# Performance work log

Hardware: AMD Instinct MI355X
Metric: run time of the kernel (lower is better)

## Reference

```python
import jax, jax.numpy as jnp
import numpy as np

N = 50000          # nodes
E = 800000         # edges (before self loops)
IN_C = 128
HEADS = 4
D = 64             # out_per_head
HID = HEADS * D    # 256
OUT_C = 128
NEG_SLOPE = 0.2


def setup_inputs() -> dict:
    key = jax.random.key(0)
    ks = jax.random.split(key, 20)
    x = jax.random.normal(ks[0], (N, IN_C), dtype=jnp.float32)
    edge_index = jax.random.randint(ks[1], (2, E), 0, N, dtype=jnp.int32)
    s = 0.05
    params = {}
    dims = [IN_C, HID, HID]
    for i in range(3):
        params[f"W{i+1}"] = jax.random.normal(ks[2 + 4 * i], (dims[i], HID), dtype=jnp.float32) * s
        params[f"a_src{i+1}"] = jax.random.normal(ks[3 + 4 * i], (HEADS, D), dtype=jnp.float32) * s
        params[f"a_dst{i+1}"] = jax.random.normal(ks[4 + 4 * i], (HEADS, D), dtype=jnp.float32) * s
        params[f"b{i+1}"] = jnp.zeros((HID,), dtype=jnp.float32)
    params["head_W"] = jax.random.normal(ks[14], (HID, OUT_C), dtype=jnp.float32) * s
    params["head_b"] = jnp.zeros((OUT_C,), dtype=jnp.float32)
    return {"x": x, "edge_index": edge_index, **params}


def _gat_layer(x, src, dst, W, a_src, a_dst, b):
    # project: [N, heads, D]
    h = (x @ W).reshape(-1, HEADS, D)
    # per-node attention halves: [N, heads]
    alpha_s = jnp.einsum("nhd,hd->nh", h, a_src)
    alpha_d = jnp.einsum("nhd,hd->nh", h, a_dst)
    # per-edge logits: [E, heads]
    logits = jax.nn.leaky_relu(alpha_s[src] + alpha_d[dst], negative_slope=NEG_SLOPE)
    # segment softmax over incoming edges of each dst node
    seg_max = jax.ops.segment_max(logits, dst, num_segments=N)
    e = jnp.exp(logits - seg_max[dst])
    seg_sum = jax.ops.segment_sum(e, dst, num_segments=N)
    alpha = e / (seg_sum[dst] + 1e-16)
    # weighted messages, scatter-aggregate: [N, heads, D]
    msg = h[src] * alpha[:, :, None]
    out = jax.ops.segment_sum(msg, dst, num_segments=N)
    return out.reshape(-1, HID) + b


def reference(x, edge_index, W1, a_src1, a_dst1, b1, W2, a_src2, a_dst2, b2,
              W3, a_src3, a_dst3, b3, head_W, head_b):
    # add self loops once (add_self_loops=True in every GATConv)
    loop = jnp.arange(N, dtype=edge_index.dtype)
    src = jnp.concatenate([edge_index[0], loop])
    dst = jnp.concatenate([edge_index[1], loop])
    h = x
    layers = [(W1, a_src1, a_dst1, b1), (W2, a_src2, a_dst2, b2), (W3, a_src3, a_dst3, b3)]
    for (W, a_s, a_d, b) in layers:
        h = jax.nn.elu(_gat_layer(h, src, dst, W, a_s, a_d, b))
        # dropout inactive in eval mode
    graph_emb = jnp.mean(h, axis=0)          # global_mean_pool over single graph
    logits = graph_emb @ head_W + head_b     # [OUT_C]
    return logits
```

## Files before the change

kernel.cpp:

```cpp
#include <hip/hip_runtime.h>
#include <stdint.h>

#define NN 50000
#define EE 800000
#define ET 850000
#define INC 128
#define HID 256
#define OUTC 128
#define NB ((NN + 255) / 256)
#define GDEG ((ET + 255) / 256)
#define GTRP 640

typedef __attribute__((ext_vector_type(4))) float f32x4;
typedef __attribute__((ext_vector_type(8))) short s16x8;
typedef __attribute__((ext_vector_type(4))) short s16x4;

static __device__ __forceinline__ float b2f(unsigned short u){
  union { float f; unsigned int i; } v; v.i = ((unsigned int)u) << 16; return v.f;
}
static __device__ __forceinline__ unsigned short f2b(float f){
  union { float f; unsigned int i; } v; v.f = f;
  unsigned int r = v.i + 0x7FFFu + ((v.i >> 16) & 1u);
  return (unsigned short)(r >> 16);
}

__global__ void k_init(const int* __restrict__ ei, int* __restrict__ cnt,
                       const float* __restrict__ W1, const float* __restrict__ W2,
                       const float* __restrict__ W3, unsigned short* __restrict__ T1,
                       unsigned short* __restrict__ T2, unsigned short* __restrict__ T3,
                       float* __restrict__ pool){
  int b = blockIdx.x, tid = threadIdx.x;
  if (b < GDEG){
    int e = b * 256 + tid;
    if (e < ET){
      int d = (e < EE) ? ei[EE + e] : (e - EE);
      atomicAdd(&cnt[d], 1);
    }
  } else if (b < GDEG + GTRP){
    int bb = b - GDEG;
    const float* W; unsigned short* WT; int K, base;
    if (bb < 128)      { W = W1; WT = T1; K = 128; base = 0; }
    else if (bb < 384) { W = W2; WT = T2; K = 256; base = 128; }
    else               { W = W3; WT = T3; K = 256; base = 384; }
    int idx = (bb - base) * 256 + tid;
    int k = idx >> 8, c = idx & 255;
    WT[c * K + k] = f2b(W[idx]);
  } else {
    pool[tid] = 0.f;
  }
}

__global__ void k_blockscan(int* __restrict__ cnt, int* __restrict__ off,
                            int* __restrict__ bsum){
  __shared__ int s[256];
  int b = blockIdx.x, tid = threadIdx.x;
  int i = b * 256 + tid;
  int v = (i < NN) ? cnt[i] : 0;
  if (i < NN) cnt[i] = 0;
  s[tid] = v; __syncthreads();
  #pragma unroll
  for (int o = 1; o < 256; o <<= 1){
    int t = (tid >= o) ? s[tid - o] : 0; __syncthreads();
    s[tid] += t; __syncthreads();
  }
  if (i < NN) off[i] = s[tid] - v;
  if (tid == 255) bsum[b] = s[255];
}

__global__ void k_scanb(const int* __restrict__ bsum, int* __restrict__ bbase){
  __shared__ int s[256];
  int tid = threadIdx.x;
  int v = (tid < NB) ? bsum[tid] : 0;
  s[tid] = v; __syncthreads();
  #pragma unroll
  for (int o = 1; o < 256; o <<= 1){
    int t = (tid >= o) ? s[tid - o] : 0; __syncthreads();
    s[tid] += t; __syncthreads();
  }
  if (tid < NB) bbase[tid] = s[tid] - v;
}

__global__ void k_scatter(const int* __restrict__ ei, const int* __restrict__ off,
                          const int* __restrict__ bbase, int* __restrict__ cnt,
                          int* __restrict__ ssrc){
  int e = blockIdx.x * 256 + threadIdx.x;
  if (e >= ET) return;
  int s, d;
  if (e < EE){ s = ei[e]; d = ei[EE + e]; } else { s = e - EE; d = s; }
  int p = off[d] + bbase[d >> 8] + atomicAdd(&cnt[d], 1);
  ssrc[p] = s;
}

template<bool AF32>
__global__ __launch_bounds__(256) void k_gemm_fused(const void* __restrict__ Av,
    const unsigned short* __restrict__ WT,
    const float* __restrict__ a_src, const float* __restrict__ a_dst,
    unsigned short* __restrict__ C, float* __restrict__ as_, float* __restrict__ ad_,
    int M, int K){
  __shared__ unsigned short sA[2][32][72];
  int tid = threadIdx.x;
  int wave = tid >> 6, lane = tid & 63;
  int bm0 = blockIdx.x * 32;
  int wc0 = wave * 64;
  f32x4 acc[2][4];
  #pragma unroll
  for (int i = 0; i < 2; i++)
    #pragma unroll
    for (int j = 0; j < 4; j++) acc[i][j] = (f32x4){0.f, 0.f, 0.f, 0.f};

  s16x8 rg;
  int r0 = tid >> 3, kb0 = (tid & 7) * 8;

  auto ldA = [&](int k0){
    int gr = bm0 + r0;
    if constexpr (AF32){
      const float* A = (const float*)Av;
      unsigned short t[8] = {0,0,0,0,0,0,0,0};
      if (gr < M){
        const float4* p = (const float4*)(A + (size_t)gr * K + k0 + kb0);
        float4 v0 = p[0], v1 = p[1];
        t[0]=f2b(v0.x); t[1]=f2b(v0.y); t[2]=f2b(v0.z); t[3]=f2b(v0.w);
        t[4]=f2b(v1.x); t[5]=f2b(v1.y); t[6]=f2b(v1.z); t[7]=f2b(v1.w);
      }
      rg = *(s16x8*)t;
    } else {
      const unsigned short* A = (const unsigned short*)Av;
      s16x8 v = (s16x8){0,0,0,0,0,0,0,0};
      if (gr < M) v = *(const s16x8*)(A + (size_t)gr * K + k0 + kb0);
      rg = v;
    }
  };

  int T = K >> 6;
  ldA(0); *(s16x8*)&sA[0][r0][kb0] = rg;
  __syncthreads();
  for (int t = 0; t < T; t++){
    int k0 = t << 6;
    if (t + 1 < T) ldA(k0 + 64);
    int cur = t & 1;
    s16x8 af[2][2], bf[2][4];
    #pragma unroll
    for (int half = 0; half < 2; half++){
      int kl = half * 32 + (lane >> 4) * 8;
      af[half][0] = *(const s16x8*)&sA[cur][lane & 15][kl];
      af[half][1] = *(const s16x8*)&sA[cur][16 + (lane & 15)][kl];
      #pragma unroll
      for (int ni = 0; ni < 4; ni++)
        bf[half][ni] = *(const s16x8*)(WT + (size_t)(wc0 + ni * 16 + (lane & 15)) * K + k0 + kl);
    }
    #pragma unroll
    for (int half = 0; half < 2; half++)
      #pragma unroll
      for (int mi = 0; mi < 2; mi++)
        #pragma unroll
        for (int ni = 0; ni < 4; ni++)
          acc[mi][ni] = __builtin_amdgcn_mfma_f32_16x16x32_bf16(af[half][mi], bf[half][ni], acc[mi][ni], 0, 0, 0);
    if (t + 1 < T) *(s16x8*)&sA[cur ^ 1][r0][kb0] = rg;
    __syncthreads();
  }

  #pragma unroll
  for (int mi = 0; mi < 2; mi++){
    #pragma unroll
    for (int ni = 0; ni < 4; ni++){
      int col = wc0 + ni * 16 + (lane & 15);
      int rb = mi * 16 + (lane >> 4) * 4;
      #pragma unroll
      for (int r = 0; r < 4; r++){
        int row = rb + r;
        if (bm0 + row < M) C[(size_t)(bm0 + row) * HID + col] = f2b(acc[mi][ni][r]);
      }
    }
  }
  float asv[4], adv[4];
  #pragma unroll
  for (int ni = 0; ni < 4; ni++){
    int d = wc0 + ni * 16 + (lane & 15);
    asv[ni] = a_src[d];
    adv[ni] = a_dst[d];
  }
  #pragma unroll
  for (int mi = 0; mi < 2; mi++){
    #pragma unroll
    for (int r = 0; r < 4; r++){
      float ps = 0.f, pd = 0.f;
      #pragma unroll
      for (int ni = 0; ni < 4; ni++){
        float cv = acc[mi][ni][r];
        ps += cv * asv[ni];
        pd += cv * adv[ni];
      }
      #pragma unroll
      for (int m = 1; m < 16; m <<= 1){
        ps += __shfl_xor(ps, m, 64);
        pd += __shfl_xor(pd, m, 64);
      }
      int row = bm0 + mi * 16 + (lane >> 4) * 4 + r;
      if ((lane & 15) == 0 && row < M){
        as_[(size_t)row * 4 + wave] = ps;
        ad_[(size_t)row * 4 + wave] = pd;
      }
    }
  }
}

__global__ __launch_bounds__(256) void k_aggregate(const int* __restrict__ off,
    const int* __restrict__ bbase, const int* __restrict__ ssrc,
    const float* __restrict__ as_, const float* __restrict__ ad_,
    const unsigned short* __restrict__ h, const float* __restrict__ bias,
    unsigned short* __restrict__ out){
  int gid = blockIdx.x * 256 + threadIdx.x;
  int wid = gid >> 6, lane = gid & 63;
  if (wid >= NN) return;
  int start = off[wid] + bbase[wid >> 8];
  int end = (wid + 1 < NN) ? (off[wid + 1] + bbase[(wid + 1) >> 8]) : ET;
  int e1 = end - 1;
  int hq = lane >> 4;
  int hh = lane & 3;
  int el = lane >> 2;
  float ad_hh = ad_[(size_t)wid * 4 + hh];
  float ssum = 0.f;
  f32x4 acc = {0.f, 0.f, 0.f, 0.f};

  for (int base = start; base < end; base += 16){
    int nv = end - base; if (nv > 16) nv = 16;
    int sidx = ssrc[min(base + el, e1)];
    float lg = as_[(size_t)sidx * 4 + hh] + ad_hh;
    lg = fmaxf(lg, 0.2f * lg);
    float w = (el < nv) ? __expf(lg) : 0.f;
    int idxs[16];
    #pragma unroll
    for (int j = 0; j < 16; j++) idxs[j] = __shfl(sidx, j * 4, 64);
    s16x4 rows[16];
    #pragma unroll
    for (int j = 0; j < 16; j++){
      if (j < nv) rows[j] = *(const s16x4*)(h + (size_t)idxs[j] * HID + lane * 4);
    }
    #pragma unroll
    for (int j = 0; j < 16; j++){
      if (j < nv){
        float wj = __shfl(w, j * 4 + hq, 64);
        ssum += wj;
        #pragma unroll
        for (int c = 0; c < 4; c++) acc[c] += wj * b2f((unsigned short)rows[j][c]);
      }
    }
  }

  float inv = 1.f / (ssum + 1e-16f);
  float4 bv = *(const float4*)(bias + lane * 4);
  float o0 = acc[0] * inv + bv.x;
  float o1 = acc[1] * inv + bv.y;
  float o2 = acc[2] * inv + bv.z;
  float o3 = acc[3] * inv + bv.w;
  o0 = o0 > 0.f ? o0 : (__expf(o0) - 1.f);
  o1 = o1 > 0.f ? o1 : (__expf(o1) - 1.f);
  o2 = o2 > 0.f ? o2 : (__expf(o2) - 1.f);
  o3 = o3 > 0.f ? o3 : (__expf(o3) - 1.f);
  s16x4 ov;
  ov[0] = (short)f2b(o0); ov[1] = (short)f2b(o1);
  ov[2] = (short)f2b(o2); ov[3] = (short)f2b(o3);
  *(s16x4*)(out + (size_t)wid * HID + lane * 4) = ov;
}

__global__ __launch_bounds__(256) void k_pool(const unsigned short* __restrict__ X,
                                              float* __restrict__ pool){
  int b = blockIdx.x, c = threadIdx.x;
  int n0 = b * 64, n1 = min(n0 + 64, NN);
  float acc = 0.f;
  for (int n = n0; n < n1; n++) acc += b2f(X[(size_t)n * HID + c]);
  atomicAdd(&pool[c], acc);
}

__global__ void k_head(const float* __restrict__ pool, const float* __restrict__ hW,
                       const float* __restrict__ hb, float* __restrict__ outp){
  int o = threadIdx.x;
  float acc = hb[o];
  const float invN = 1.f / (float)NN;
  for (int c = 0; c < HID; c++) acc += pool[c] * invN * hW[c * OUTC + o];
  outp[o] = acc;
}

extern "C" void kernel_launch(void* const* d_in, const int* in_sizes, int n_in,
                              void* d_out, int out_size, void* d_ws, size_t ws_size,
                              hipStream_t stream){
  const float* x  = (const float*)d_in[0];
  const int* ei   = (const int*)d_in[1];
  const float* W[3]   = {(const float*)d_in[2],  (const float*)d_in[6],  (const float*)d_in[10]};
  const float* Asr[3] = {(const float*)d_in[3],  (const float*)d_in[7],  (const float*)d_in[11]};
  const float* Adt[3] = {(const float*)d_in[4],  (const float*)d_in[8],  (const float*)d_in[12]};
  const float* B[3]   = {(const float*)d_in[5],  (const float*)d_in[9],  (const float*)d_in[13]};
  const float* hW = (const float*)d_in[14];
  const float* hb = (const float*)d_in[15];

  char* w = (char*)d_ws; size_t o = 0;
  auto alloc = [&](size_t b) -> void* { void* p = w + o; o = (o + b + 255) & ~(size_t)255; return p; };
  int* cnt  = (int*)alloc((size_t)NN * 4);
  int* off  = (int*)alloc((size_t)NN * 4);
  int* ssrc = (int*)alloc((size_t)ET * 4);
  int* bsum = (int*)alloc((size_t)NB * 4);
  int* bbase= (int*)alloc((size_t)NB * 4);
  unsigned short* hbuf = (unsigned short*)alloc((size_t)NN * HID * 2);
  float* as_ = (float*)alloc((size_t)NN * 4 * 4);
  float* ad_ = (float*)alloc((size_t)NN * 4 * 4);
  unsigned short* X0 = (unsigned short*)alloc((size_t)NN * HID * 2);
  unsigned short* X1 = (unsigned short*)alloc((size_t)NN * HID * 2);
  unsigned short* WT1 = (unsigned short*)alloc((size_t)INC * HID * 2);
  unsigned short* WT2 = (unsigned short*)alloc((size_t)HID * HID * 2);
  unsigned short* WT3 = (unsigned short*)alloc((size_t)HID * HID * 2);
  float* pool = (float*)alloc(256 * 4);

  hipMemsetAsync(cnt, 0, (size_t)NN * 4, stream);
  k_init<<<GDEG + GTRP + 1, 256, 0, stream>>>(ei, cnt, W[0], W[1], W[2], WT1, WT2, WT3, pool);
  k_blockscan<<<NB, 256, 0, stream>>>(cnt, off, bsum);
  k_scanb<<<1, 256, 0, stream>>>(bsum, bbase);
  k_scatter<<<GDEG, 256, 0, stream>>>(ei, off, bbase, cnt, ssrc);

  const unsigned short* WTs[3] = {WT1, WT2, WT3};
  unsigned short* outbuf[3] = {X0, X1, X0};
  int Ks[3] = {INC, HID, HID};
  const void* Ain = (const void*)x;
  int gB = (NN + 63) / 64;
  int gG = (NN + 31) / 32;
  int gW = (NN * 64 + 255) / 256;
  for (int l = 0; l < 3; l++){
    if (l == 0) k_gemm_fused<true ><<<gG, 256, 0, stream>>>(Ain, WTs[l], Asr[l], Adt[l], hbuf, as_, ad_, NN, Ks[l]);
    else        k_gemm_fused<false><<<gG, 256, 0, stream>>>(Ain, WTs[l], Asr[l], Adt[l], hbuf, as_, ad_, NN, Ks[l]);
    k_aggregate<<<gW, 256, 0, stream>>>(off, bbase, ssrc, as_, ad_, hbuf, B[l], outbuf[l]);
    Ain = (const void*)outbuf[l];
  }
  k_pool<<<gB, 256, 0, stream>>>(X0, pool);
  k_head<<<1, 128, 0, stream>>>(pool, hW, hb, (float*)d_out);
}
```

Measured before the change: 441.1 us.

## Software-pipeline aggregation over two nodes per wave and record CSR slot in init

```diff
diff --git a/kernel.cpp b/kernel.cpp
--- a/kernel.cpp
+++ b/kernel.cpp
@@ -25,6 +25,7 @@
 }
 
 __global__ void k_init(const int* __restrict__ ei, int* __restrict__ cnt,
+                       int* __restrict__ pos,
                        const float* __restrict__ W1, const float* __restrict__ W2,
                        const float* __restrict__ W3, unsigned short* __restrict__ T1,
                        unsigned short* __restrict__ T2, unsigned short* __restrict__ T3,
@@ -34,7 +35,7 @@
     int e = b * 256 + tid;
     if (e < ET){
       int d = (e < EE) ? ei[EE + e] : (e - EE);
-      atomicAdd(&cnt[d], 1);
+      pos[e] = atomicAdd(&cnt[d], 1);
     }
   } else if (b < GDEG + GTRP){
     int bb = b - GDEG;
@@ -50,13 +51,12 @@
   }
 }
 
-__global__ void k_blockscan(int* __restrict__ cnt, int* __restrict__ off,
+__global__ void k_blockscan(const int* __restrict__ cnt, int* __restrict__ off,
                             int* __restrict__ bsum){
   __shared__ int s[256];
   int b = blockIdx.x, tid = threadIdx.x;
   int i = b * 256 + tid;
   int v = (i < NN) ? cnt[i] : 0;
-  if (i < NN) cnt[i] = 0;
   s[tid] = v; __syncthreads();
   #pragma unroll
   for (int o = 1; o < 256; o <<= 1){
@@ -81,14 +81,13 @@
 }
 
 __global__ void k_scatter(const int* __restrict__ ei, const int* __restrict__ off,
-                          const int* __restrict__ bbase, int* __restrict__ cnt,
+                          const int* __restrict__ bbase, const int* __restrict__ pos,
                           int* __restrict__ ssrc){
   int e = blockIdx.x * 256 + threadIdx.x;
   if (e >= ET) return;
   int s, d;
   if (e < EE){ s = ei[e]; d = ei[EE + e]; } else { s = e - EE; d = s; }
-  int p = off[d] + bbase[d >> 8] + atomicAdd(&cnt[d], 1);
-  ssrc[p] = s;
+  ssrc[off[d] + bbase[d >> 8] + pos[e]] = s;
 }
 
 template<bool AF32>
@@ -204,63 +203,134 @@
   }
 }
 
-__global__ __launch_bounds__(256) void k_aggregate(const int* __restrict__ off,
+struct NS {
+  int p, end, e1;
+  int j0, j1, j2, j3, j4, j5, j6, j7;
+  s16x4 r0, r1, r2, r3;
+  float a0, a1, a2, a3;
+  float ad2, s0, s1;
+  f32x4 A, B, C, D;
+};
+
+__global__ __launch_bounds__(64) void k_aggregate(const int* __restrict__ off,
     const int* __restrict__ bbase, const int* __restrict__ ssrc,
     const float* __restrict__ as_, const float* __restrict__ ad_,
     const unsigned short* __restrict__ h, const float* __restrict__ bias,
     unsigned short* __restrict__ out){
-  int gid = blockIdx.x * 256 + threadIdx.x;
-  int wid = gid >> 6, lane = gid & 63;
-  if (wid >= NN) return;
-  int start = off[wid] + bbase[wid >> 8];
-  int end = (wid + 1 < NN) ? (off[wid + 1] + bbase[(wid + 1) >> 8]) : ET;
-  int e1 = end - 1;
+  int lane = threadIdx.x;
+  int widA = blockIdx.x * 2, widB = widA + 1;
   int hq = lane >> 4;
-  int hh = lane & 3;
-  int el = lane >> 2;
-  float ad_hh = ad_[(size_t)wid * 4 + hh];
-  float ssum = 0.f;
-  f32x4 acc = {0.f, 0.f, 0.f, 0.f};
-
-  for (int base = start; base < end; base += 16){
-    int nv = end - base; if (nv > 16) nv = 16;
-    int sidx = ssrc[min(base + el, e1)];
-    float lg = as_[(size_t)sidx * 4 + hh] + ad_hh;
-    lg = fmaxf(lg, 0.2f * lg);
-    float w = (el < nv) ? __expf(lg) : 0.f;
-    int idxs[16];
-    #pragma unroll
-    for (int j = 0; j < 16; j++) idxs[j] = __shfl(sidx, j * 4, 64);
-    s16x4 rows[16];
-    #pragma unroll
-    for (int j = 0; j < 16; j++){
-      if (j < nv) rows[j] = *(const s16x4*)(h + (size_t)idxs[j] * HID + lane * 4);
-    }
-    #pragma unroll
-    for (int j = 0; j < 16; j++){
-      if (j < nv){
-        float wj = __shfl(w, j * 4 + hq, 64);
-        ssum += wj;
-        #pragma unroll
-        for (int c = 0; c < 4; c++) acc[c] += wj * b2f((unsigned short)rows[j][c]);
-      }
-    }
-  }
-
-  float inv = 1.f / (ssum + 1e-16f);
+
+  auto ns_init = [&](NS& n, int wid){
+    n.p = off[wid] + bbase[wid >> 8];
+    n.end = (wid + 1 < NN) ? (off[wid + 1] + bbase[(wid + 1) >> 8]) : ET;
+    n.e1 = n.end - 1;
+    n.ad2 = ad_[(size_t)wid * 4 + hq];
+    n.s0 = 0.f; n.s1 = 0.f;
+    n.A = (f32x4){0,0,0,0}; n.B = (f32x4){0,0,0,0};
+    n.C = (f32x4){0,0,0,0}; n.D = (f32x4){0,0,0,0};
+    n.j0 = ssrc[n.p];
+    n.j1 = ssrc[min(n.p + 1, n.e1)]; n.j2 = ssrc[min(n.p + 2, n.e1)];
+    n.j3 = ssrc[min(n.p + 3, n.e1)];
+    n.j4 = ssrc[min(n.p + 4, n.e1)]; n.j5 = ssrc[min(n.p + 5, n.e1)];
+    n.j6 = ssrc[min(n.p + 6, n.e1)]; n.j7 = ssrc[min(n.p + 7, n.e1)];
+    n.r0 = *(const s16x4*)(h + (size_t)n.j0 * HID + lane * 4);
+    n.r1 = *(const s16x4*)(h + (size_t)n.j1 * HID + lane * 4);
+    n.r2 = *(const s16x4*)(h + (size_t)n.j2 * HID + lane * 4);
+    n.r3 = *(const s16x4*)(h + (size_t)n.j3 * HID + lane * 4);
+    n.a0 = as_[(size_t)n.j0 * 4 + hq]; n.a1 = as_[(size_t)n.j1 * 4 + hq];
+    n.a2 = as_[(size_t)n.j2 * 4 + hq]; n.a3 = as_[(size_t)n.j3 * 4 + hq];
+  };
+
+  auto ns_step = [&](NS& n, bool clamp){
+    s16x4 u0 = *(const s16x4*)(h + (size_t)n.j4 * HID + lane * 4);
+    s16x4 u1 = *(const s16x4*)(h + (size_t)n.j5 * HID + lane * 4);
+    s16x4 u2 = *(const s16x4*)(h + (size_t)n.j6 * HID + lane * 4);
+    s16x4 u3 = *(const s16x4*)(h + (size_t)n.j7 * HID + lane * 4);
+    float b0 = as_[(size_t)n.j4 * 4 + hq], b1 = as_[(size_t)n.j5 * 4 + hq];
+    float b2 = as_[(size_t)n.j6 * 4 + hq], b3 = as_[(size_t)n.j7 * 4 + hq];
+    int t0, t1, t2, t3;
+    if (clamp){
+      t0 = ssrc[min(n.p + 8, n.e1)];  t1 = ssrc[min(n.p + 9, n.e1)];
+      t2 = ssrc[min(n.p + 10, n.e1)]; t3 = ssrc[min(n.p + 11, n.e1)];
+    } else {
+      t0 = ssrc[n.p + 8]; t1 = ssrc[n.p + 9]; t2 = ssrc[n.p + 10]; t3 = ssrc[n.p + 11];
+    }
+    float l0 = n.a0 + n.ad2; l0 = fmaxf(l0, 0.2f * l0);
+    float l1 = n.a1 + n.ad2; l1 = fmaxf(l1, 0.2f * l1);
+    float l2 = n.a2 + n.ad2; l2 = fmaxf(l2, 0.2f * l2);
+    float l3 = n.a3 + n.ad2; l3 = fmaxf(l3, 0.2f * l3);
+    float w0 = __expf(l0), w1 = __expf(l1), w2 = __expf(l2), w3 = __expf(l3);
+    n.s0 += w0 + w2; n.s1 += w1 + w3;
+    #pragma unroll
+    for (int c = 0; c < 4; c++){
+      n.A[c] += w0 * b2f((unsigned short)n.r0[c]);
+      n.B[c] += w1 * b2f((unsigned short)n.r1[c]);
+      n.C[c] += w2 * b2f((unsigned short)n.r2[c]);
+      n.D[c] += w3 * b2f((unsigned short)n.r3[c]);
+    }
+    n.j0 = n.j4; n.j1 = n.j5; n.j2 = n.j6; n.j3 = n.j7;
+    n.j4 = t0; n.j5 = t1; n.j6 = t2; n.j7 = t3;
+    n.r0 = u0; n.r1 = u1; n.r2 = u2; n.r3 = u3;
+    n.a0 = b0; n.a1 = b1; n.a2 = b2; n.a3 = b3;
+    n.p += 4;
+  };
+
+  auto ns_tail = [&](NS& n){
+    int rem = n.end - n.p;
+    if (rem > 0){
+      float l = n.a0 + n.ad2; l = fmaxf(l, 0.2f * l);
+      float w = __expf(l); n.s0 += w;
+      #pragma unroll
+      for (int c = 0; c < 4; c++) n.A[c] += w * b2f((unsigned short)n.r0[c]);
+    }
+    if (rem > 1){
+      float l = n.a1 + n.ad2; l = fmaxf(l, 0.2f * l);
+      float w = __expf(l); n.s1 += w;
+      #pragma unroll
+      for (int c = 0; c < 4; c++) n.B[c] += w * b2f((unsigned short)n.r1[c]);
+    }
+    if (rem > 2){
+      float l = n.a2 + n.ad2; l = fmaxf(l, 0.2f * l);
+      float w = __expf(l); n.s0 += w;
+      #pragma unroll
+      for (int c = 0; c < 4; c++) n.C[c] += w * b2f((unsigned short)n.r2[c]);
+    }
+  };
+
   float4 bv = *(const float4*)(bias + lane * 4);
-  float o0 = acc[0] * inv + bv.x;
-  float o1 = acc[1] * inv + bv.y;
-  float o2 = acc[2] * inv + bv.z;
-  float o3 = acc[3] * inv + bv.w;
-  o0 = o0 > 0.f ? o0 : (__expf(o0) - 1.f);
-  o1 = o1 > 0.f ? o1 : (__expf(o1) - 1.f);
-  o2 = o2 > 0.f ? o2 : (__expf(o2) - 1.f);
-  o3 = o3 > 0.f ? o3 : (__expf(o3) - 1.f);
-  s16x4 ov;
-  ov[0] = (short)f2b(o0); ov[1] = (short)f2b(o1);
-  ov[2] = (short)f2b(o2); ov[3] = (short)f2b(o3);
-  *(s16x4*)(out + (size_t)wid * HID + lane * 4) = ov;
+  auto ns_emit = [&](NS& n, int wid){
+    float inv = 1.f / (n.s0 + n.s1 + 1e-16f);
+    float o0 = (n.A[0] + n.B[0] + n.C[0] + n.D[0]) * inv + bv.x;
+    float o1 = (n.A[1] + n.B[1] + n.C[1] + n.D[1]) * inv + bv.y;
+    float o2 = (n.A[2] + n.B[2] + n.C[2] + n.D[2]) * inv + bv.z;
+    float o3 = (n.A[3] + n.B[3] + n.C[3] + n.D[3]) * inv + bv.w;
+    o0 = o0 > 0.f ? o0 : (__expf(o0) - 1.f);
+    o1 = o1 > 0.f ? o1 : (__expf(o1) - 1.f);
+    o2 = o2 > 0.f ? o2 : (__expf(o2) - 1.f);
+    o3 = o3 > 0.f ? o3 : (__expf(o3) - 1.f);
+    s16x4 ov;
+    ov[0] = (short)f2b(o0); ov[1] = (short)f2b(o1);
+    ov[2] = (short)f2b(o2); ov[3] = (short)f2b(o3);
+    *(s16x4*)(out + (size_t)wid * HID + lane * 4) = ov;
+  };
+
+  NS na, nb;
+  ns_init(na, widA);
+  ns_init(nb, widB);
+
+  while (na.p + 11 < na.end && nb.p + 11 < nb.end){
+    ns_step(na, false);
+    ns_step(nb, false);
+  }
+  while (na.p + 11 < na.end) ns_step(na, false);
+  while (na.p + 3 < na.end)  ns_step(na, true);
+  ns_tail(na);
+  ns_emit(na, widA);
+  while (nb.p + 11 < nb.end) ns_step(nb, false);
+  while (nb.p + 3 < nb.end)  ns_step(nb, true);
+  ns_tail(nb);
+  ns_emit(nb, widB);
 }
 
 __global__ __launch_bounds__(256) void k_pool(const unsigned short* __restrict__ X,
@@ -298,6 +368,7 @@
   int* cnt  = (int*)alloc((size_t)NN * 4);
   int* off  = (int*)alloc((size_t)NN * 4);
   int* ssrc = (int*)alloc((size_t)ET * 4);
+  int* pos  = (int*)alloc((size_t)ET * 4);
   int* bsum = (int*)alloc((size_t)NB * 4);
   int* bbase= (int*)alloc((size_t)NB * 4);
   unsigned short* hbuf = (unsigned short*)alloc((size_t)NN * HID * 2);
@@ -311,10 +382,10 @@
   float* pool = (float*)alloc(256 * 4);
 
   hipMemsetAsync(cnt, 0, (size_t)NN * 4, stream);
-  k_init<<<GDEG + GTRP + 1, 256, 0, stream>>>(ei, cnt, W[0], W[1], W[2], WT1, WT2, WT3, pool);
+  k_init<<<GDEG + GTRP + 1, 256, 0, stream>>>(ei, cnt, pos, W[0], W[1], W[2], WT1, WT2, WT3, pool);
   k_blockscan<<<NB, 256, 0, stream>>>(cnt, off, bsum);
   k_scanb<<<1, 256, 0, stream>>>(bsum, bbase);
-  k_scatter<<<GDEG, 256, 0, stream>>>(ei, off, bbase, cnt, ssrc);
+  k_scatter<<<GDEG, 256, 0, stream>>>(ei, off, bbase, pos, ssrc);
 
   const unsigned short* WTs[3] = {WT1, WT2, WT3};
   unsigned short* outbuf[3] = {X0, X1, X0};
@@ -322,11 +393,10 @@
   const void* Ain = (const void*)x;
   int gB = (NN + 63) / 64;
   int gG = (NN + 31) / 32;
-  int gW = (NN * 64 + 255) / 256;
   for (int l = 0; l < 3; l++){
     if (l == 0) k_gemm_fused<true ><<<gG, 256, 0, stream>>>(Ain, WTs[l], Asr[l], Adt[l], hbuf, as_, ad_, NN, Ks[l]);
     else        k_gemm_fused<false><<<gG, 256, 0, stream>>>(Ain, WTs[l], Asr[l], Adt[l], hbuf, as_, ad_, NN, Ks[l]);
-    k_aggregate<<<gW, 256, 0, stream>>>(off, bbase, ssrc, as_, ad_, hbuf, B[l], outbuf[l]);
+    k_aggregate<<<NN / 2, 64, 0, stream>>>(off, bbase, ssrc, as_, ad_, hbuf, B[l], outbuf[l]);
     Ain = (const void*)outbuf[l];
   }
   k_pool<<<gB, 256, 0, stream>>>(X0, pool);
```

New measurement: 396.9 us. -10.0%, faster.
